# Kernel tuning notes

Hardware: AMD Instinct MI355X
Metric: run time of the kernel (lower is better)

Reference implementation:

```python
import jax, jax.numpy as jnp
import numpy as np

B, T_FEAT, D = 16, 4096, 512
T_TOK = 1024


def setup_inputs() -> dict:
    key = jax.random.key(0)
    k1, k2, k3, k4, k5 = jax.random.split(key, 5)
    encoded_feats = jax.random.normal(k1, (B, T_FEAT, D), dtype=jnp.float32)
    encoded_feat_lengths = jax.random.randint(k2, (B,), 1, T_FEAT + 1).astype(jnp.int32)
    asr_token_ids = jax.random.randint(k3, (B, T_TOK), 0, 32000).astype(jnp.int64)
    asr_token_lengths = jax.random.randint(k4, (B,), 1, T_TOK + 1).astype(jnp.int32)
    # fractional [start, end] alignments in [0,1], sorted so start <= end
    asr_token_alignments = jnp.sort(jax.random.uniform(k5, (B, T_TOK, 2), dtype=jnp.float32), axis=-1)
    return {
        "encoded_feats": encoded_feats,
        "encoded_feat_lengths": encoded_feat_lengths,
        "asr_token_ids": asr_token_ids,
        "asr_token_lengths": asr_token_lengths,
        "asr_token_alignments": asr_token_alignments,
    }


def reference(encoded_feats, encoded_feat_lengths, asr_token_ids, asr_token_lengths, asr_token_alignments):
    # alignments: fractional positions scaled to frame indices, truncated like torch .int()
    align = (asr_token_alignments * encoded_feat_lengths[:, None, None].astype(jnp.float32)).astype(jnp.int32)  # [B, Tt, 2]
    idx = jnp.arange(encoded_feats.shape[1], dtype=jnp.int32)  # [Tf]
    # token validity mask (~make_pad_mask)
    token_mask = jnp.arange(asr_token_ids.shape[1], dtype=jnp.int32)[None, :] < asr_token_lengths[:, None]  # [B, Tt]
    # [B, Tt, Tf] segment membership mask (inclusive [start, end])
    mask = token_mask[:, :, None] & (idx[None, None, :] >= align[:, :, 0:1]) & (idx[None, None, :] <= align[:, :, 1:2])
    maskf = mask.astype(encoded_feats.dtype)
    # masked sum without materializing [B, Tt, Tf, D]
    sums = jnp.einsum("btf,bfd->btd", maskf, encoded_feats)  # [B, Tt, D]
    counts = jnp.sum(maskf, axis=-1, keepdims=True)  # [B, Tt, 1]
    segmented_feats = jnp.nan_to_num(sums / counts)
    return segmented_feats, asr_token_lengths
```

## Files before the change

kernel.cpp:

```cpp
#include <hip/hip_runtime.h>
#include <hip/hip_fp16.h>

namespace {

constexpr int kB  = 16;
constexpr int kF  = 4096;
constexpr int kD  = 512;
constexpr int kTT = 1024;
constexpr int kC  = 64;
constexpr int kD4 = kD / 4;

__device__ inline void acc4(float4& a, const float4& v) {
    a.x += v.x; a.y += v.y; a.z += v.z; a.w += v.w;
}

__device__ inline ushort4 pack_h4(const float4& v) {
    ushort4 u;
    u.x = __half_as_ushort(__float2half_rn(v.x));
    u.y = __half_as_ushort(__float2half_rn(v.y));
    u.z = __half_as_ushort(__float2half_rn(v.z));
    u.w = __half_as_ushort(__float2half_rn(v.w));
    return u;
}

__device__ inline float4 unpack_h4(const ushort4& u) {
    return make_float4(__half2float(__ushort_as_half(u.x)),
                       __half2float(__ushort_as_half(u.y)),
                       __half2float(__ushort_as_half(u.z)),
                       __half2float(__ushort_as_half(u.w)));
}

__global__ void chunk_prefix_k(const float4* __restrict__ feats,
                               const int* __restrict__ flens,
                               ushort4* __restrict__ Pc,
                               float4* __restrict__ S) {
    int tid = blockIdx.x * blockDim.x + threadIdx.x;
    int q = tid & (kD4 - 1);
    int c = (tid >> 7) & (kC - 1);
    int b = tid >> 13;
    int flen = flens[b];
    int base_row = c * 64;
    float4 r = make_float4(0.f, 0.f, 0.f, 0.f);
    int nval = flen - base_row;
    size_t fbase = ((size_t)(b * kF + base_row)) * kD4 + q;
    if (nval > 0) {
        if (nval > 64) nval = 64;
        const float4* p = feats + fbase;
        ushort4* o = Pc + fbase;
        if (nval == 64) {
#pragma unroll 8
            for (int i = 0; i < 64; ++i) {
                acc4(r, p[(size_t)i * kD4]);
                o[(size_t)i * kD4] = pack_h4(r);
            }
        } else {
            for (int i = 0; i < nval; ++i) {
                acc4(r, p[(size_t)i * kD4]);
                o[(size_t)i * kD4] = pack_h4(r);
            }
        }
    }
    S[((size_t)(b * kC + c)) * kD4 + q] = r;
}

__global__ void chunk_offsets_k(const float* __restrict__ S,
                                float* __restrict__ O64) {
    int tid = blockIdx.x * blockDim.x + threadIdx.x;
    int d = tid & (kD - 1);
    int b = tid >> 9;
    float r = 0.f;
    for (int c = 0; c < kC; ++c) {
        O64[((size_t)(b * kC + c)) * kD + d] = r;
        r += S[((size_t)(b * kC + c)) * kD + d];
    }
}

__device__ inline float4 prefix_at(const ushort4* __restrict__ Pc,
                                   const float4* __restrict__ O64,
                                   int b, int r, int q) {
    float4 acc = O64[((size_t)(b * kC + (r >> 6))) * kD4 + q];
    float4 p = unpack_h4(Pc[((size_t)(b * kF + r)) * kD4 + q]);
    acc4(acc, p);
    return acc;
}

__global__ void gather_k(const ushort4* __restrict__ Pc,
                         const float4* __restrict__ O64,
                         const int* __restrict__ flens,
                         const int* __restrict__ tlens,
                         const float2* __restrict__ aligns,
                         float4* __restrict__ out,
                         float* __restrict__ out_lens) {
    int blk = blockIdx.x;
    int t = blk & (kTT - 1);
    int b = blk >> 10;
    int q = threadIdx.x;
    int tlen = tlens[b];
    int flen = flens[b];
    float fl = (float)flen;
    float2 a = aligns[blk];
    int s = (int)(a.x * fl);
    int e = (int)(a.y * fl);
    if (e > kF - 1) e = kF - 1;
    int cnt = e - s + 1;
    float4 res = make_float4(0.f, 0.f, 0.f, 0.f);
    if (t < tlen && cnt > 0 && s < kF) {
        int er = e;      if (er > flen - 1) er = flen - 1;
        float4 hi = prefix_at(Pc, O64, b, er, q);
        float4 lo = make_float4(0.f, 0.f, 0.f, 0.f);
        if (s > 0) {
            int sr = s - 1; if (sr > flen - 1) sr = flen - 1;
            lo = prefix_at(Pc, O64, b, sr, q);
        }
        float fc = (float)cnt;
        res = make_float4((hi.x - lo.x) / fc, (hi.y - lo.y) / fc,
                          (hi.z - lo.z) / fc, (hi.w - lo.w) / fc);
    }
    out[((size_t)blk) * kD4 + q] = res;
    if (t == 0 && q == 0) out_lens[b] = (float)tlen;
}

__global__ void direct_k(const float4* __restrict__ feats,
                         const int* __restrict__ flens,
                         const int* __restrict__ tlens,
                         const float2* __restrict__ aligns,
                         float4* __restrict__ out,
                         float* __restrict__ out_lens) {
    int blk = blockIdx.x;
    int t = blk & (kTT - 1);
    int b = blk >> 10;
    int q = threadIdx.x;
    int tlen = tlens[b];
    float fl = (float)flens[b];
    float2 a = aligns[blk];
    int s = (int)(a.x * fl);
    int e = (int)(a.y * fl);
    if (e > kF - 1) e = kF - 1;
    int cnt = e - s + 1;
    float4 res = make_float4(0.f, 0.f, 0.f, 0.f);
    if (t < tlen && cnt > 0 && s < kF) {
        const float4* p = feats + ((size_t)(b * kF + s)) * kD4 + q;
        float4 r = make_float4(0.f, 0.f, 0.f, 0.f);
        for (int i = 0; i < cnt; ++i) acc4(r, p[(size_t)i * kD4]);
        float fc = (float)cnt;
        res = make_float4(r.x / fc, r.y / fc, r.z / fc, r.w / fc);
    }
    out[((size_t)blk) * kD4 + q] = res;
    if (t == 0 && q == 0) out_lens[b] = (float)tlen;
}

}

extern "C" void kernel_launch(void* const* d_in, const int* in_sizes, int n_in,
                              void* d_out, int out_size, void* d_ws, size_t ws_size,
                              hipStream_t stream) {
    const float4* feats  = (const float4*)d_in[0];
    const int*    flens  = (const int*)d_in[1];
    const int*    tlens  = (const int*)d_in[3];
    const float2* aligns = (const float2*)d_in[4];

    float* out      = (float*)d_out;
    float* out_lens = out + (size_t)kB * kTT * kD;

    const size_t needPc  = (size_t)kB * kF * kD * sizeof(unsigned short);
    const size_t needS   = (size_t)kB * kC * kD * sizeof(float);
    const size_t needO64 = needS;

    if (ws_size >= needPc + needS + needO64) {
        ushort4* Pc  = (ushort4*)d_ws;
        float4*  S   = (float4*)((char*)d_ws + needPc);
        float4*  O64 = (float4*)((char*)d_ws + needPc + needS);

        int n1 = kB * kC * kD4;
        chunk_prefix_k<<<n1 / 256, 256, 0, stream>>>(feats, flens, Pc, S);
        int n2 = kB * kD;
        chunk_offsets_k<<<n2 / 256, 256, 0, stream>>>((const float*)S, (float*)O64);
        gather_k<<<kB * kTT, kD4, 0, stream>>>(Pc, O64, flens, tlens, aligns,
                                               (float4*)out, out_lens);
    } else {
        direct_k<<<kB * kTT, kD4, 0, stream>>>(feats, flens, tlens, aligns,
                                               (float4*)out, out_lens);
    }
}
```

Measured before the change: 41.34 us.

## Halve prefix chunk size, drop chunk-sum buffer, pack two tokens per gather block

```diff
diff --git a/kernel.cpp b/kernel.cpp
--- a/kernel.cpp
+++ b/kernel.cpp
@@ -7,13 +7,13 @@
 constexpr int kF  = 4096;
 constexpr int kD  = 512;
 constexpr int kTT = 1024;
-constexpr int kC  = 64;
+constexpr int kSC = 32;
+constexpr int kNC = kF / kSC;
 constexpr int kD4 = kD / 4;
 
 __device__ inline void acc4(float4& a, const float4& v) {
     a.x += v.x; a.y += v.y; a.z += v.z; a.w += v.w;
 }
-
 __device__ inline ushort4 pack_h4(const float4& v) {
     ushort4 u;
     u.x = __half_as_ushort(__float2half_rn(v.x));
@@ -22,7 +22,6 @@
     u.w = __half_as_ushort(__float2half_rn(v.w));
     return u;
 }
-
 __device__ inline float4 unpack_h4(const ushort4& u) {
     return make_float4(__half2float(__ushort_as_half(u.x)),
                        __half2float(__ushort_as_half(u.y)),
@@ -30,71 +29,71 @@
                        __half2float(__ushort_as_half(u.w)));
 }
 
-__global__ void chunk_prefix_k(const float4* __restrict__ feats,
-                               const int* __restrict__ flens,
-                               ushort4* __restrict__ Pc,
-                               float4* __restrict__ S) {
+__global__ __launch_bounds__(256) void chunk_prefix_k(
+    const float4* __restrict__ feats,
+    const int* __restrict__ flens,
+    ushort4* __restrict__ Pc) {
     int tid = blockIdx.x * blockDim.x + threadIdx.x;
     int q = tid & (kD4 - 1);
-    int c = (tid >> 7) & (kC - 1);
-    int b = tid >> 13;
+    int c = (tid >> 7) & (kNC - 1);
+    int b = tid >> 14;
     int flen = flens[b];
-    int base_row = c * 64;
+    int base = c * kSC;
+    int nval = flen - base;
+    if (nval <= 0) return;
+    if (nval > kSC) nval = kSC;
+    size_t fbase = ((size_t)(b * kF + base)) * kD4 + q;
+    const float4* p = feats + fbase;
+    ushort4* o = Pc + fbase;
     float4 r = make_float4(0.f, 0.f, 0.f, 0.f);
-    int nval = flen - base_row;
-    size_t fbase = ((size_t)(b * kF + base_row)) * kD4 + q;
-    if (nval > 0) {
-        if (nval > 64) nval = 64;
-        const float4* p = feats + fbase;
-        ushort4* o = Pc + fbase;
-        if (nval == 64) {
+    if (nval == kSC) {
 #pragma unroll 8
-            for (int i = 0; i < 64; ++i) {
-                acc4(r, p[(size_t)i * kD4]);
-                o[(size_t)i * kD4] = pack_h4(r);
-            }
-        } else {
-            for (int i = 0; i < nval; ++i) {
-                acc4(r, p[(size_t)i * kD4]);
-                o[(size_t)i * kD4] = pack_h4(r);
-            }
+        for (int i = 0; i < kSC; ++i) {
+            acc4(r, p[(size_t)i * kD4]);
+            o[(size_t)i * kD4] = pack_h4(r);
         }
-    }
-    S[((size_t)(b * kC + c)) * kD4 + q] = r;
-}
-
-__global__ void chunk_offsets_k(const float* __restrict__ S,
-                                float* __restrict__ O64) {
-    int tid = blockIdx.x * blockDim.x + threadIdx.x;
-    int d = tid & (kD - 1);
-    int b = tid >> 9;
-    float r = 0.f;
-    for (int c = 0; c < kC; ++c) {
-        O64[((size_t)(b * kC + c)) * kD + d] = r;
-        r += S[((size_t)(b * kC + c)) * kD + d];
+    } else {
+        for (int i = 0; i < nval; ++i) {
+            acc4(r, p[(size_t)i * kD4]);
+            o[(size_t)i * kD4] = pack_h4(r);
+        }
     }
 }
 
-__device__ inline float4 prefix_at(const ushort4* __restrict__ Pc,
-                                   const float4* __restrict__ O64,
-                                   int b, int r, int q) {
-    float4 acc = O64[((size_t)(b * kC + (r >> 6))) * kD4 + q];
-    float4 p = unpack_h4(Pc[((size_t)(b * kF + r)) * kD4 + q]);
-    acc4(acc, p);
-    return acc;
+__global__ __launch_bounds__(256) void chunk_offsets_k(
+    const unsigned short* __restrict__ PcH,
+    const int* __restrict__ flens,
+    float* __restrict__ O) {
+    int gid = blockIdx.x * blockDim.x + threadIdx.x;
+    int d = gid & (kD - 1);
+    int b = gid >> 9;
+    int flen = flens[b];
+    float r = 0.f;
+#pragma unroll 8
+    for (int c = 0; c < kNC; ++c) {
+        O[((size_t)(b * kNC + c)) * kD + d] = r;
+        int start = c * kSC;
+        if (start < flen) {
+            int last = start + kSC - 1;
+            if (last > flen - 1) last = flen - 1;
+            r += __half2float(__ushort_as_half(PcH[((size_t)(b * kF + last)) * kD + d]));
+        }
+    }
 }
 
-__global__ void gather_k(const ushort4* __restrict__ Pc,
-                         const float4* __restrict__ O64,
-                         const int* __restrict__ flens,
-                         const int* __restrict__ tlens,
-                         const float2* __restrict__ aligns,
-                         float4* __restrict__ out,
-                         float* __restrict__ out_lens) {
-    int blk = blockIdx.x;
+__global__ __launch_bounds__(256) void gather_k(
+    const ushort4* __restrict__ Pc4,
+    const float4* __restrict__ O4,
+    const int* __restrict__ flens,
+    const int* __restrict__ tlens,
+    const float2* __restrict__ aligns,
+    float4* __restrict__ out,
+    float* __restrict__ out_lens) {
+    int q = threadIdx.x & 127;
+    int which = threadIdx.x >> 7;
+    int blk = blockIdx.x * 2 + which;
     int t = blk & (kTT - 1);
     int b = blk >> 10;
-    int q = threadIdx.x;
     int tlen = tlens[b];
     int flen = flens[b];
     float fl = (float)flen;
@@ -106,12 +105,19 @@
     float4 res = make_float4(0.f, 0.f, 0.f, 0.f);
     if (t < tlen && cnt > 0 && s < kF) {
         int er = e;      if (er > flen - 1) er = flen - 1;
-        float4 hi = prefix_at(Pc, O64, b, er, q);
+        int sr = s - 1;  if (sr > flen - 1) sr = flen - 1;
+        bool haveLo = (s > 0);
+        float4  oHi = O4[((size_t)(b * kNC + (er >> 5))) * kD4 + q];
+        ushort4 pHi = Pc4[((size_t)(b * kF + er)) * kD4 + q];
+        float4  oLo = make_float4(0.f, 0.f, 0.f, 0.f);
+        ushort4 pLo = make_ushort4(0, 0, 0, 0);
+        if (haveLo) {
+            oLo = O4[((size_t)(b * kNC + (sr >> 5))) * kD4 + q];
+            pLo = Pc4[((size_t)(b * kF + sr)) * kD4 + q];
+        }
+        float4 hi = unpack_h4(pHi); acc4(hi, oHi);
         float4 lo = make_float4(0.f, 0.f, 0.f, 0.f);
-        if (s > 0) {
-            int sr = s - 1; if (sr > flen - 1) sr = flen - 1;
-            lo = prefix_at(Pc, O64, b, sr, q);
-        }
+        if (haveLo) { lo = unpack_h4(pLo); acc4(lo, oLo); }
         float fc = (float)cnt;
         res = make_float4((hi.x - lo.x) / fc, (hi.y - lo.y) / fc,
                           (hi.z - lo.z) / fc, (hi.w - lo.w) / fc);
@@ -162,21 +168,19 @@
     float* out      = (float*)d_out;
     float* out_lens = out + (size_t)kB * kTT * kD;
 
-    const size_t needPc  = (size_t)kB * kF * kD * sizeof(unsigned short);
-    const size_t needS   = (size_t)kB * kC * kD * sizeof(float);
-    const size_t needO64 = needS;
+    const size_t needPc = (size_t)kB * kF * kD * sizeof(unsigned short);
+    const size_t needO  = (size_t)kB * kNC * kD * sizeof(float);
 
-    if (ws_size >= needPc + needS + needO64) {
-        ushort4* Pc  = (ushort4*)d_ws;
-        float4*  S   = (float4*)((char*)d_ws + needPc);
-        float4*  O64 = (float4*)((char*)d_ws + needPc + needS);
+    if (ws_size >= needPc + needO) {
+        ushort4* Pc = (ushort4*)d_ws;
+        float*   O  = (float*)((char*)d_ws + needPc);
 
-        int n1 = kB * kC * kD4;
-        chunk_prefix_k<<<n1 / 256, 256, 0, stream>>>(feats, flens, Pc, S);
-        int n2 = kB * kD;
-        chunk_offsets_k<<<n2 / 256, 256, 0, stream>>>((const float*)S, (float*)O64);
-        gather_k<<<kB * kTT, kD4, 0, stream>>>(Pc, O64, flens, tlens, aligns,
-                                               (float4*)out, out_lens);
+        int n1 = kB * kNC * kD4;
+        chunk_prefix_k<<<n1 / 256, 256, 0, stream>>>(feats, flens, Pc);
+        chunk_offsets_k<<<(kB * kD) / 256, 256, 0, stream>>>(
+            (const unsigned short*)Pc, flens, O);
+        gather_k<<<(kB * kTT) / 2, 256, 0, stream>>>(
+            Pc, (const float4*)O, flens, tlens, aligns, (float4*)out, out_lens);
     } else {
         direct_k<<<kB * kTT, kD4, 0, stream>>>(feats, flens, tlens, aligns,
                                                (float4*)out, out_lens);
```

Measured after the change: 67.69 us. 1.64x slower.

## Fuse chunk-offset scan into gather kernel using shared-memory offsets

Applied to the files above, without the earlier changes.

```diff
diff --git a/kernel.cpp b/kernel.cpp
--- a/kernel.cpp
+++ b/kernel.cpp
@@ -8,12 +8,16 @@
 constexpr int kD  = 512;
 constexpr int kTT = 1024;
 constexpr int kC  = 64;
+constexpr int kCL = kF / kC;
 constexpr int kD4 = kD / 4;
+constexpr int kDG = 128;
+constexpr int kNDG = kD / kDG;
+constexpr int kTS = 16;
+constexpr int kTokPerBlk = kTT / kTS;
 
 __device__ inline void acc4(float4& a, const float4& v) {
     a.x += v.x; a.y += v.y; a.z += v.z; a.w += v.w;
 }
-
 __device__ inline ushort4 pack_h4(const float4& v) {
     ushort4 u;
     u.x = __half_as_ushort(__float2half_rn(v.x));
@@ -23,33 +27,27 @@
     return u;
 }
 
-__device__ inline float4 unpack_h4(const ushort4& u) {
-    return make_float4(__half2float(__ushort_as_half(u.x)),
-                       __half2float(__ushort_as_half(u.y)),
-                       __half2float(__ushort_as_half(u.z)),
-                       __half2float(__ushort_as_half(u.w)));
-}
-
-__global__ void chunk_prefix_k(const float4* __restrict__ feats,
-                               const int* __restrict__ flens,
-                               ushort4* __restrict__ Pc,
-                               float4* __restrict__ S) {
+__global__ __launch_bounds__(256) void chunk_prefix_k(
+    const float4* __restrict__ feats,
+    const int* __restrict__ flens,
+    ushort4* __restrict__ Pc,
+    float4* __restrict__ S) {
     int tid = blockIdx.x * blockDim.x + threadIdx.x;
     int q = tid & (kD4 - 1);
     int c = (tid >> 7) & (kC - 1);
     int b = tid >> 13;
     int flen = flens[b];
-    int base_row = c * 64;
+    int base_row = c * kCL;
     float4 r = make_float4(0.f, 0.f, 0.f, 0.f);
     int nval = flen - base_row;
     size_t fbase = ((size_t)(b * kF + base_row)) * kD4 + q;
     if (nval > 0) {
-        if (nval > 64) nval = 64;
+        if (nval > kCL) nval = kCL;
         const float4* p = feats + fbase;
         ushort4* o = Pc + fbase;
-        if (nval == 64) {
+        if (nval == kCL) {
 #pragma unroll 8
-            for (int i = 0; i < 64; ++i) {
+            for (int i = 0; i < kCL; ++i) {
                 acc4(r, p[(size_t)i * kD4]);
                 o[(size_t)i * kD4] = pack_h4(r);
             }
@@ -63,61 +61,66 @@
     S[((size_t)(b * kC + c)) * kD4 + q] = r;
 }
 
-__global__ void chunk_offsets_k(const float* __restrict__ S,
-                                float* __restrict__ O64) {
-    int tid = blockIdx.x * blockDim.x + threadIdx.x;
-    int d = tid & (kD - 1);
-    int b = tid >> 9;
-    float r = 0.f;
-    for (int c = 0; c < kC; ++c) {
-        O64[((size_t)(b * kC + c)) * kD + d] = r;
-        r += S[((size_t)(b * kC + c)) * kD + d];
+__global__ __launch_bounds__(256) void gather_scan_k(
+    const unsigned short* __restrict__ PcH,
+    const float* __restrict__ Sf,
+    const int* __restrict__ flens,
+    const int* __restrict__ tlens,
+    const float2* __restrict__ aligns,
+    float* __restrict__ out,
+    float* __restrict__ out_lens) {
+    __shared__ float Olds[kC][kDG];
+
+    const int bid = blockIdx.x;
+    const int ts = bid & (kTS - 1);
+    const int dg = (bid >> 4) & (kNDG - 1);
+    const int b  = bid >> 6;
+    const int tid = threadIdx.x;
+    const int flen = flens[b];
+    const int tlen = tlens[b];
+
+    if (tid < kDG) {
+        int d = dg * kDG + tid;
+        float r = 0.f;
+#pragma unroll 8
+        for (int cc = 0; cc < kC; ++cc) {
+            Olds[cc][tid] = r;
+            r += Sf[((size_t)(b * kC + cc)) * kD + d];
+        }
     }
-}
+    __syncthreads();
 
-__device__ inline float4 prefix_at(const ushort4* __restrict__ Pc,
-                                   const float4* __restrict__ O64,
-                                   int b, int r, int q) {
-    float4 acc = O64[((size_t)(b * kC + (r >> 6))) * kD4 + q];
-    float4 p = unpack_h4(Pc[((size_t)(b * kF + r)) * kD4 + q]);
-    acc4(acc, p);
-    return acc;
-}
+    const int q = tid & (kDG - 1);
+    const int which = tid >> 7;
+    const float fl = (float)flen;
+    const int dbase = dg * kDG + q;
+    const int tok0 = ts * kTokPerBlk;
 
-__global__ void gather_k(const ushort4* __restrict__ Pc,
-                         const float4* __restrict__ O64,
-                         const int* __restrict__ flens,
-                         const int* __restrict__ tlens,
-                         const float2* __restrict__ aligns,
-                         float4* __restrict__ out,
-                         float* __restrict__ out_lens) {
-    int blk = blockIdx.x;
-    int t = blk & (kTT - 1);
-    int b = blk >> 10;
-    int q = threadIdx.x;
-    int tlen = tlens[b];
-    int flen = flens[b];
-    float fl = (float)flen;
-    float2 a = aligns[blk];
-    int s = (int)(a.x * fl);
-    int e = (int)(a.y * fl);
-    if (e > kF - 1) e = kF - 1;
-    int cnt = e - s + 1;
-    float4 res = make_float4(0.f, 0.f, 0.f, 0.f);
-    if (t < tlen && cnt > 0 && s < kF) {
-        int er = e;      if (er > flen - 1) er = flen - 1;
-        float4 hi = prefix_at(Pc, O64, b, er, q);
-        float4 lo = make_float4(0.f, 0.f, 0.f, 0.f);
-        if (s > 0) {
-            int sr = s - 1; if (sr > flen - 1) sr = flen - 1;
-            lo = prefix_at(Pc, O64, b, sr, q);
+    for (int k = 0; k < kTokPerBlk; k += 2) {
+        int t = tok0 + k + which;
+        float2 a = aligns[b * kTT + t];
+        int s = (int)(a.x * fl);
+        int e = (int)(a.y * fl);
+        if (e > kF - 1) e = kF - 1;
+        int cnt = e - s + 1;
+        float res = 0.f;
+        if (t < tlen && cnt > 0 && s < kF) {
+            int er = e;     if (er > flen - 1) er = flen - 1;
+            float hi = Olds[er >> 6][q] +
+                       __half2float(__ushort_as_half(
+                           PcH[((size_t)(b * kF + er)) * kD + dbase]));
+            float lo = 0.f;
+            if (s > 0) {
+                int sr = s - 1; if (sr > flen - 1) sr = flen - 1;
+                lo = Olds[sr >> 6][q] +
+                     __half2float(__ushort_as_half(
+                         PcH[((size_t)(b * kF + sr)) * kD + dbase]));
+            }
+            res = (hi - lo) / (float)cnt;
         }
-        float fc = (float)cnt;
-        res = make_float4((hi.x - lo.x) / fc, (hi.y - lo.y) / fc,
-                          (hi.z - lo.z) / fc, (hi.w - lo.w) / fc);
+        out[((size_t)(b * kTT + t)) * kD + dbase] = res;
     }
-    out[((size_t)blk) * kD4 + q] = res;
-    if (t == 0 && q == 0) out_lens[b] = (float)tlen;
+    if (ts == 0 && dg == 0 && tid == 0) out_lens[b] = (float)tlen;
 }
 
 __global__ void direct_k(const float4* __restrict__ feats,
@@ -162,21 +165,20 @@
     float* out      = (float*)d_out;
     float* out_lens = out + (size_t)kB * kTT * kD;
 
-    const size_t needPc  = (size_t)kB * kF * kD * sizeof(unsigned short);
-    const size_t needS   = (size_t)kB * kC * kD * sizeof(float);
-    const size_t needO64 = needS;
+    const size_t needPc = (size_t)kB * kF * kD * sizeof(unsigned short);
+    const size_t needS  = (size_t)kB * kC * kD * sizeof(float);
 
-    if (ws_size >= needPc + needS + needO64) {
-        ushort4* Pc  = (ushort4*)d_ws;
-        float4*  S   = (float4*)((char*)d_ws + needPc);
-        float4*  O64 = (float4*)((char*)d_ws + needPc + needS);
+    if (ws_size >= needPc + needS) {
+        ushort4* Pc = (ushort4*)d_ws;
+        float4*  S  = (float4*)((char*)d_ws + needPc);
 
         int n1 = kB * kC * kD4;
         chunk_prefix_k<<<n1 / 256, 256, 0, stream>>>(feats, flens, Pc, S);
-        int n2 = kB * kD;
-        chunk_offsets_k<<<n2 / 256, 256, 0, stream>>>((const float*)S, (float*)O64);
-        gather_k<<<kB * kTT, kD4, 0, stream>>>(Pc, O64, flens, tlens, aligns,
-                                               (float4*)out, out_lens);
+
+        int ngather = kB * kNDG * kTS;
+        gather_scan_k<<<ngather, 256, 0, stream>>>(
+            (const unsigned short*)Pc, (const float*)S, flens, tlens, aligns,
+            out, out_lens);
     } else {
         direct_k<<<kB * kTT, kD4, 0, stream>>>(feats, flens, tlens, aligns,
                                                (float4*)out, out_lens);
```

Result: slower. 57.58 us (+39.3%).
